# Kernel optimization log

Hardware: AMD Instinct MI355X
Metric: run time of the kernel (lower is better)

Reference implementation:

```python
import jax, jax.numpy as jnp
import numpy as np

TOP_K = 2


def setup_inputs() -> dict:
    key = jax.random.key(0)
    k1, k2, k3, k4, k5 = jax.random.split(key, 5)
    B, S, H, F, E = 2, 2048, 1024, 4096, 8
    scale = 0.02
    return {
        "hidden_states": jax.random.normal(k1, (B, S, H), dtype=jnp.float32),
        "w_gate": jax.random.normal(k2, (H, E), dtype=jnp.float32) * scale,
        "w_gate_proj": jax.random.normal(k3, (E, H, F), dtype=jnp.float32) * scale,
        "w_up_proj": jax.random.normal(k4, (E, H, F), dtype=jnp.float32) * scale,
        "w_down_proj": jax.random.normal(k5, (E, F, H), dtype=jnp.float32) * scale,
    }


def reference(hidden_states, w_gate, w_gate_proj, w_up_proj, w_down_proj):
    B, S, H = hidden_states.shape
    E = w_gate_proj.shape[0]
    x = hidden_states.reshape(-1, H)  # [T, H]

    # Router: softmax in float32, then top-k (NOT renormalized, matching source).
    router_logits = x @ w_gate  # [T, E]
    routing_probs = jax.nn.softmax(router_logits.astype(jnp.float32), axis=-1)
    routing_weights, selected_experts = jax.lax.top_k(routing_probs, TOP_K)  # [T, k]
    routing_weights = routing_weights.astype(x.dtype)

    out = jnp.zeros_like(x)
    # Small fixed loop over experts; per-token weight is zero for unrouted
    # tokens, so the masked dense computation is mathematically identical to
    # the gather/index_add dispatch in the source.
    for e in range(E):
        w_e = jnp.sum(routing_weights * (selected_experts == e), axis=-1)  # [T]
        h = jax.nn.silu(x @ w_gate_proj[e]) * (x @ w_up_proj[e])  # [T, F]
        out = out + (h @ w_down_proj[e]) * w_e[:, None]
    return out.reshape(B, S, H)
```

## Files before the change

kernel.cpp:

```cpp
#include <hip/hip_runtime.h>
#include <hip/hip_bf16.h>

#define T_TOK 4096
#define HDIM  1024
#define FDIM  4096
#define NEXP  8
#define CAP   4096
#define MAXWL 128
#define OBR   (2 * T_TOK + 128)

typedef __attribute__((ext_vector_type(8))) short short8;
typedef __attribute__((ext_vector_type(4))) float floatx4;
typedef __attribute__((ext_vector_type(4))) float float4v;
typedef __attribute__((ext_vector_type(4))) unsigned short ushort4v;

__device__ __forceinline__ unsigned short f2bf(float f) {
    union { float f; unsigned int u; } v; v.f = f;
    unsigned int u = v.u;
    u += 0x7fffu + ((u >> 16) & 1u);
    return (unsigned short)(u >> 16);
}

__device__ __forceinline__ void gl2lds16(const void* g, void* l) {
    __builtin_amdgcn_global_load_lds(
        (const __attribute__((address_space(1))) unsigned int*)g,
        (__attribute__((address_space(3))) unsigned int*)l,
        16, 0, 0);
}

__global__ void k_transpose_cast(const float* __restrict__ src, unsigned short* __restrict__ dst,
                                 int R, int C) {
    __shared__ float tile[64][65];
    size_t base = (size_t)blockIdx.z * (size_t)R * (size_t)C;
    int c0 = blockIdx.x * 64, r0 = blockIdx.y * 64;
    int lx = threadIdx.x & 15, ly = threadIdx.x >> 4;
#pragma unroll
    for (int i = 0; i < 4; ++i) {
        int rr = i * 16 + ly;
        float4v v = *(const float4v*)(src + base + (size_t)(r0 + rr) * C + c0 + lx * 4);
        tile[rr][lx * 4 + 0] = v[0]; tile[rr][lx * 4 + 1] = v[1];
        tile[rr][lx * 4 + 2] = v[2]; tile[rr][lx * 4 + 3] = v[3];
    }
    __syncthreads();
#pragma unroll
    for (int i = 0; i < 4; ++i) {
        int cc = i * 16 + ly;
        ushort4v o = { f2bf(tile[lx * 4 + 0][cc]), f2bf(tile[lx * 4 + 1][cc]),
                       f2bf(tile[lx * 4 + 2][cc]), f2bf(tile[lx * 4 + 3][cc]) };
        *(ushort4v*)(dst + base + (size_t)(c0 + cc) * R + r0 + lx * 4) = o;
    }
}

__global__ void k_router(const float* __restrict__ x, const float* __restrict__ wgate,
                         unsigned short* __restrict__ xb,
                         int* __restrict__ counts, int* __restrict__ ltok,
                         float* __restrict__ lwt, int* __restrict__ tslot) {
    int lane = threadIdx.x & 63;
    int tok = blockIdx.x * 4 + (threadIdx.x >> 6);
    const float* xr = x + (size_t)tok * HDIM;
    unsigned short* xbr = xb + (size_t)tok * HDIM;
    float acc[NEXP];
#pragma unroll
    for (int e = 0; e < NEXP; ++e) acc[e] = 0.f;
    for (int it = 0; it < HDIM / 256; ++it) {
        int h0 = it * 256 + lane * 4;
        float4v xv = *(const float4v*)(xr + h0);
        ushort4v xo = { f2bf(xv[0]), f2bf(xv[1]), f2bf(xv[2]), f2bf(xv[3]) };
        *(ushort4v*)(xbr + h0) = xo;
#pragma unroll
        for (int j = 0; j < 4; ++j) {
            float4v w0 = *(const float4v*)(wgate + (size_t)(h0 + j) * NEXP);
            float4v w1 = *(const float4v*)(wgate + (size_t)(h0 + j) * NEXP + 4);
            float xs = xv[j];
            acc[0] += xs * w0[0]; acc[1] += xs * w0[1];
            acc[2] += xs * w0[2]; acc[3] += xs * w0[3];
            acc[4] += xs * w1[0]; acc[5] += xs * w1[1];
            acc[6] += xs * w1[2]; acc[7] += xs * w1[3];
        }
    }
#pragma unroll
    for (int off = 32; off >= 1; off >>= 1)
#pragma unroll
        for (int e = 0; e < NEXP; ++e)
            acc[e] += __shfl_xor(acc[e], off, 64);
    if (lane == 0) {
        float m = acc[0];
#pragma unroll
        for (int e = 1; e < NEXP; ++e) m = fmaxf(m, acc[e]);
        float p[NEXP], s = 0.f;
#pragma unroll
        for (int e = 0; e < NEXP; ++e) { p[e] = __expf(acc[e] - m); s += p[e]; }
        float inv = 1.f / s;
#pragma unroll
        for (int e = 0; e < NEXP; ++e) p[e] *= inv;
        int e0 = 0; float b0 = p[0];
#pragma unroll
        for (int e = 1; e < NEXP; ++e) if (p[e] > b0) { b0 = p[e]; e0 = e; }
        int e1 = -1; float b1 = -1.f;
#pragma unroll
        for (int e = 0; e < NEXP; ++e) if (e != e0 && p[e] > b1) { b1 = p[e]; e1 = e; }
        int p0 = atomicAdd(&counts[e0], 1);
        ltok[e0 * CAP + p0] = tok; lwt[e0 * CAP + p0] = b0;
        int p1 = atomicAdd(&counts[e1], 1);
        ltok[e1 * CAP + p1] = tok; lwt[e1 * CAP + p1] = b1;
        tslot[tok * 2]     = (e0 << 16) | p0;
        tslot[tok * 2 + 1] = (e1 << 16) | p1;
    }
}

__global__ void k_prefix(const int* __restrict__ counts, int* __restrict__ offs,
                         int* __restrict__ wl, int* __restrict__ nwl) {
    if (threadIdx.x == 0) {
        int s = 0;
#pragma unroll
        for (int e = 0; e < NEXP; ++e) { offs[e] = s; s += counts[e]; }
        int n = 0;
        for (int e = 0; e < NEXP; ++e)
            for (int r = 0; r * 128 < counts[e] && n < MAXWL; ++r)
                wl[n++] = (e << 8) | r;
        nwl[0] = n;
    }
}

__global__ __launch_bounds__(256, 4)
void k_gemm1(const unsigned short* __restrict__ xb,
             const unsigned short* __restrict__ wgt,
             const unsigned short* __restrict__ wut,
             const int* __restrict__ counts, const int* __restrict__ offs,
             const int* __restrict__ ltok,
             const int* __restrict__ wl, const int* __restrict__ nwl,
             unsigned short* __restrict__ hbuf)
{
    if ((int)blockIdx.y >= nwl[0]) return;
    const int w = wl[blockIdx.y];
    const int e = w >> 8, rowtile = w & 255;
    const int M = counts[e];
    const int ftile = blockIdx.x;

    __shared__ __align__(16) unsigned short lA[128 * 32];
    __shared__ __align__(16) unsigned short lBg[64 * 32];
    __shared__ __align__(16) unsigned short lBu[64 * 32];
    __shared__ int stok[128];

    const int t = threadIdx.x;
    const int wave = t >> 6, lane = t & 63;

    if (t < 128) {
        int i = rowtile * 128 + t;
        stok[t] = (i < M) ? ltok[e * CAP + i] : ltok[e * CAP];
    }
    __syncthreads();

    const int r0 = t >> 2, k8 = t & 3;
    const unsigned short* pA0 = xb + (size_t)stok[r0] * HDIM + k8 * 8;
    const unsigned short* pA1 = xb + (size_t)stok[r0 + 64] * HDIM + k8 * 8;
    const size_t wbase = (size_t)e * FDIM * HDIM + (size_t)(ftile * 64) * HDIM;
    const unsigned short* pG0 = wgt + wbase + (size_t)r0 * HDIM + k8 * 8;
    const unsigned short* pU0 = wut + wbase + (size_t)r0 * HDIM + k8 * 8;

    unsigned short* dA0 = &lA[wave * 512];
    unsigned short* dA1 = &lA[2048 + wave * 512];
    unsigned short* dG0 = &lBg[wave * 512];
    unsigned short* dU0 = &lBu[wave * 512];

    const int wm = wave >> 1, wn = wave & 1;
    const int fr = lane & 15, kg = lane >> 4;

    floatx4 accg[4][2], accu[4][2];
#pragma unroll
    for (int mi = 0; mi < 4; ++mi)
#pragma unroll
        for (int ni = 0; ni < 2; ++ni) {
            floatx4 z = {0.f, 0.f, 0.f, 0.f};
            accg[mi][ni] = z; accu[mi][ni] = z;
        }

    for (int ks = 0; ks < HDIM / 32; ++ks) {
        gl2lds16(pA0, dA0); gl2lds16(pA1, dA1);
        gl2lds16(pG0, dG0); gl2lds16(pU0, dU0);
        pA0 += 32; pA1 += 32; pG0 += 32; pU0 += 32;
        __syncthreads();
        short8 a[4], bg[2], bu[2];
#pragma unroll
        for (int mi = 0; mi < 4; ++mi)
            a[mi] = *(const short8*)&lA[(wm * 64 + mi * 16 + fr) * 32 + kg * 8];
#pragma unroll
        for (int ni = 0; ni < 2; ++ni) {
            bg[ni] = *(const short8*)&lBg[(wn * 32 + ni * 16 + fr) * 32 + kg * 8];
            bu[ni] = *(const short8*)&lBu[(wn * 32 + ni * 16 + fr) * 32 + kg * 8];
        }
#pragma unroll
        for (int mi = 0; mi < 4; ++mi)
#pragma unroll
            for (int ni = 0; ni < 2; ++ni) {
                accg[mi][ni] = __builtin_amdgcn_mfma_f32_16x16x32_bf16(a[mi], bg[ni], accg[mi][ni], 0, 0, 0);
                accu[mi][ni] = __builtin_amdgcn_mfma_f32_16x16x32_bf16(a[mi], bu[ni], accu[mi][ni], 0, 0, 0);
            }
        __syncthreads();
    }

    const int hrow0 = offs[e] + rowtile * 128;
#pragma unroll
    for (int mi = 0; mi < 4; ++mi)
#pragma unroll
        for (int ni = 0; ni < 2; ++ni) {
            int c = ftile * 64 + wn * 32 + ni * 16 + fr;
#pragma unroll
            for (int r = 0; r < 4; ++r) {
                int rr = wm * 64 + mi * 16 + kg * 4 + r;
                if (rowtile * 128 + rr < M) {
                    float g = accg[mi][ni][r];
                    float val = (g / (1.f + __expf(-g))) * accu[mi][ni][r];
                    hbuf[(size_t)(hrow0 + rr) * FDIM + c] = f2bf(val);
                }
            }
        }
}

__global__ __launch_bounds__(256, 2)
void k_gemm2(const unsigned short* __restrict__ hbuf,
             const unsigned short* __restrict__ wdt,
             const int* __restrict__ counts, const int* __restrict__ offs,
             const float* __restrict__ lwt,
             const int* __restrict__ wl, const int* __restrict__ nwl,
             float* __restrict__ obuf)
{
    if ((int)blockIdx.y >= nwl[0]) return;
    const int w = wl[blockIdx.y];
    const int e = w >> 8, rowtile = w & 255;
    const int M = counts[e];
    const int htile = blockIdx.x;
    const int khalf = blockIdx.z;

    __shared__ __align__(16) unsigned short lA[128 * 32];
    __shared__ __align__(16) unsigned short lB[128 * 32];
    __shared__ float swt[128];

    const int t = threadIdx.x;
    const int wave = t >> 6, lane = t & 63;

    if (t < 128) {
        int i = rowtile * 128 + t;
        swt[t] = (i < M) ? lwt[e * CAP + i] : 0.f;
    }

    const int row0 = offs[e] + rowtile * 128;
    const int r0 = t >> 2, k8 = t & 3;
    const int kofs = khalf * (FDIM / 2);
    const unsigned short* pA0 = hbuf + (size_t)(row0 + r0) * FDIM + kofs + k8 * 8;
    const unsigned short* pA1 = hbuf + (size_t)(row0 + 64 + r0) * FDIM + kofs + k8 * 8;
    const size_t wb = (size_t)e * HDIM * FDIM + (size_t)(htile * 128) * FDIM;
    const unsigned short* pB0 = wdt + wb + (size_t)r0 * FDIM + kofs + k8 * 8;
    const unsigned short* pB1 = wdt + wb + (size_t)(64 + r0) * FDIM + kofs + k8 * 8;

    unsigned short* dA0 = &lA[wave * 512];
    unsigned short* dA1 = &lA[2048 + wave * 512];
    unsigned short* dB0 = &lB[wave * 512];
    unsigned short* dB1 = &lB[2048 + wave * 512];

    const int wm = wave >> 1, wn = wave & 1;
    const int fr = lane & 15, kg = lane >> 4;

    floatx4 acc[4][4];
#pragma unroll
    for (int mi = 0; mi < 4; ++mi)
#pragma unroll
        for (int ni = 0; ni < 4; ++ni) {
            floatx4 z = {0.f, 0.f, 0.f, 0.f};
            acc[mi][ni] = z;
        }

    for (int ks = 0; ks < FDIM / 64; ++ks) {
        gl2lds16(pA0, dA0); gl2lds16(pA1, dA1);
        gl2lds16(pB0, dB0); gl2lds16(pB1, dB1);
        pA0 += 32; pA1 += 32; pB0 += 32; pB1 += 32;
        __syncthreads();
        short8 a[4], b[4];
#pragma unroll
        for (int mi = 0; mi < 4; ++mi)
            a[mi] = *(const short8*)&lA[(wm * 64 + mi * 16 + fr) * 32 + kg * 8];
#pragma unroll
        for (int ni = 0; ni < 4; ++ni)
            b[ni] = *(const short8*)&lB[(wn * 64 + ni * 16 + fr) * 32 + kg * 8];
#pragma unroll
        for (int mi = 0; mi < 4; ++mi)
#pragma unroll
            for (int ni = 0; ni < 4; ++ni)
                acc[mi][ni] = __builtin_amdgcn_mfma_f32_16x16x32_bf16(a[mi], b[ni], acc[mi][ni], 0, 0, 0);
        __syncthreads();
    }

    float* ob = obuf + (size_t)khalf * OBR * HDIM;
#pragma unroll
    for (int mi = 0; mi < 4; ++mi)
#pragma unroll
        for (int ni = 0; ni < 4; ++ni) {
            int c = htile * 128 + wn * 64 + ni * 16 + fr;
#pragma unroll
            for (int r = 0; r < 4; ++r) {
                int rr = wm * 64 + mi * 16 + kg * 4 + r;
                if (rowtile * 128 + rr < M)
                    ob[(size_t)(row0 + rr) * HDIM + c] = acc[mi][ni][r] * swt[rr];
            }
        }
}

__global__ void k_combine(const float* __restrict__ obuf, const int* __restrict__ tslot,
                          const int* __restrict__ offs, float* __restrict__ out) {
    int gid = blockIdx.x * 256 + threadIdx.x;
    int tok = gid >> 8;
    int c = (gid & 255) * 4;
    int s0 = tslot[tok * 2], s1 = tslot[tok * 2 + 1];
    size_t r0 = (size_t)(offs[s0 >> 16] + (s0 & 0xFFFF));
    size_t r1 = (size_t)(offs[s1 >> 16] + (s1 & 0xFFFF));
    float4v v00 = *(const float4v*)(obuf + r0 * HDIM + c);
    float4v v01 = *(const float4v*)(obuf + ((size_t)OBR + r0) * HDIM + c);
    float4v v10 = *(const float4v*)(obuf + r1 * HDIM + c);
    float4v v11 = *(const float4v*)(obuf + ((size_t)OBR + r1) * HDIM + c);
    float4v s = v00 + v01 + v10 + v11;
    *(float4v*)(out + (size_t)tok * HDIM + c) = s;
}

extern "C" void kernel_launch(void* const* d_in, const int* in_sizes, int n_in,
                              void* d_out, int out_size, void* d_ws, size_t ws_size,
                              hipStream_t stream) {
    const float* x     = (const float*)d_in[0];
    const float* wgate = (const float*)d_in[1];
    const float* wg    = (const float*)d_in[2];
    const float* wu    = (const float*)d_in[3];
    const float* wd    = (const float*)d_in[4];
    float* out = (float*)d_out;

    char* ws = (char*)d_ws;
    size_t off = 0;
    unsigned short* xb  = (unsigned short*)(ws + off); off += (size_t)T_TOK * HDIM * 2;
    unsigned short* wgt = (unsigned short*)(ws + off); off += (size_t)NEXP * FDIM * HDIM * 2;
    unsigned short* wut = (unsigned short*)(ws + off); off += (size_t)NEXP * FDIM * HDIM * 2;
    unsigned short* wdt = (unsigned short*)(ws + off); off += (size_t)NEXP * HDIM * FDIM * 2;
    unsigned short* hbuf= (unsigned short*)(ws + off); off += (size_t)OBR * FDIM * 2;
    int*   ltok   = (int*)(ws + off);   off += (size_t)NEXP * CAP * 4;
    float* lwt    = (float*)(ws + off); off += (size_t)NEXP * CAP * 4;
    int*   tslot  = (int*)(ws + off);   off += (size_t)T_TOK * 2 * 4;
    int*   counts = (int*)(ws + off);   off += 256;
    int*   offs   = (int*)(ws + off);   off += 256;
    int*   wl     = (int*)(ws + off);   off += MAXWL * 4;
    int*   nwl    = (int*)(ws + off);   off += 256;
    float* obuf = (float*)wgt;

    hipMemsetAsync(counts, 0, 32, stream);

    k_router<<<T_TOK / 4, 256, 0, stream>>>(x, wgate, xb, counts, ltok, lwt, tslot);
    k_transpose_cast<<<dim3(FDIM / 64, HDIM / 64, NEXP), 256, 0, stream>>>(wg, wgt, HDIM, FDIM);
    k_transpose_cast<<<dim3(FDIM / 64, HDIM / 64, NEXP), 256, 0, stream>>>(wu, wut, HDIM, FDIM);
    k_transpose_cast<<<dim3(HDIM / 64, FDIM / 64, NEXP), 256, 0, stream>>>(wd, wdt, FDIM, HDIM);
    k_prefix<<<1, 64, 0, stream>>>(counts, offs, wl, nwl);
    k_gemm1<<<dim3(FDIM / 64, 72), 256, 0, stream>>>(xb, wgt, wut, counts, offs, ltok, wl, nwl, hbuf);
    k_gemm2<<<dim3(HDIM / 128, 72, 2), 256, 0, stream>>>(hbuf, wdt, counts, offs, lwt, wl, nwl, obuf);
    k_combine<<<T_TOK * HDIM / 1024, 256, 0, stream>>>(obuf, tslot, offs, out);
}
```

Baseline: 832.9 us.

## Rewrite gate/up GEMM with 256-row tiles, triple-buffered swizzled LDS pipeline

The first expert GEMM now uses 512-thread blocks over 256-token row tiles with a 64-wide K step. Global-to-LDS copies are triple-buffered and split into two phases that overlap with MFMA work, controlled by explicit vmcnt waits, raw barriers and setprio. LDS rows are XOR-swizzled to avoid bank conflicts. A separate 256-row worklist is built in the prefix kernel. The intent is more reuse of weight tiles and hidden load latency, at the cost of much more LDS per block and lower occupancy.

Result: slower. 879.4 us (+5.6%).

```diff
diff --git a/kernel.cpp b/kernel.cpp
--- a/kernel.cpp
+++ b/kernel.cpp
@@ -7,12 +7,17 @@
 #define NEXP  8
 #define CAP   4096
 #define MAXWL 128
+#define NT1MAX 40
 #define OBR   (2 * T_TOK + 128)
 
 typedef __attribute__((ext_vector_type(8))) short short8;
 typedef __attribute__((ext_vector_type(4))) float floatx4;
 typedef __attribute__((ext_vector_type(4))) float float4v;
 typedef __attribute__((ext_vector_type(4))) unsigned short ushort4v;
+
+#define BAR() do { asm volatile("" ::: "memory"); __builtin_amdgcn_s_barrier(); asm volatile("" ::: "memory"); } while (0)
+#define VMW6() asm volatile("s_waitcnt vmcnt(6)" ::: "memory")
+#define VMW0() asm volatile("s_waitcnt vmcnt(0)" ::: "memory")
 
 __device__ __forceinline__ unsigned short f2bf(float f) {
     union { float f; unsigned int u; } v; v.f = f;
@@ -109,7 +114,8 @@
 }
 
 __global__ void k_prefix(const int* __restrict__ counts, int* __restrict__ offs,
-                         int* __restrict__ wl, int* __restrict__ nwl) {
+                         int* __restrict__ wl, int* __restrict__ nwl,
+                         int* __restrict__ wl1, int* __restrict__ nwl1) {
     if (threadIdx.x == 0) {
         int s = 0;
 #pragma unroll
@@ -119,52 +125,64 @@
             for (int r = 0; r * 128 < counts[e] && n < MAXWL; ++r)
                 wl[n++] = (e << 8) | r;
         nwl[0] = n;
-    }
-}
-
-__global__ __launch_bounds__(256, 4)
+        int n1 = 0;
+        for (int e = 0; e < NEXP; ++e)
+            for (int r = 0; r * 256 < counts[e] && n1 < 64; ++r)
+                wl1[n1++] = (e << 8) | r;
+        nwl1[0] = n1;
+    }
+}
+
+__global__ __launch_bounds__(512, 2)
 void k_gemm1(const unsigned short* __restrict__ xb,
              const unsigned short* __restrict__ wgt,
              const unsigned short* __restrict__ wut,
              const int* __restrict__ counts, const int* __restrict__ offs,
              const int* __restrict__ ltok,
-             const int* __restrict__ wl, const int* __restrict__ nwl,
+             const int* __restrict__ wl1, const int* __restrict__ nwl1,
              unsigned short* __restrict__ hbuf)
 {
-    if ((int)blockIdx.y >= nwl[0]) return;
-    const int w = wl[blockIdx.y];
-    const int e = w >> 8, rowtile = w & 255;
+    if ((int)blockIdx.y >= nwl1[0]) return;
+    const int wle = wl1[blockIdx.y];
+    const int e = wle >> 8, rowtile = wle & 255;
     const int M = counts[e];
     const int ftile = blockIdx.x;
 
-    __shared__ __align__(16) unsigned short lA[128 * 32];
-    __shared__ __align__(16) unsigned short lBg[64 * 32];
-    __shared__ __align__(16) unsigned short lBu[64 * 32];
-    __shared__ int stok[128];
+    __shared__ __align__(16) unsigned short lA[3][256 * 64];
+    __shared__ __align__(16) unsigned short lBg[3][64 * 64];
+    __shared__ __align__(16) unsigned short lBu[3][64 * 64];
+    __shared__ int stok[256];
 
     const int t = threadIdx.x;
     const int wave = t >> 6, lane = t & 63;
-
-    if (t < 128) {
-        int i = rowtile * 128 + t;
-        stok[t] = (i < M) ? ltok[e * CAP + i] : ltok[e * CAP];
-    }
-    __syncthreads();
-
-    const int r0 = t >> 2, k8 = t & 3;
-    const unsigned short* pA0 = xb + (size_t)stok[r0] * HDIM + k8 * 8;
-    const unsigned short* pA1 = xb + (size_t)stok[r0 + 64] * HDIM + k8 * 8;
-    const size_t wbase = (size_t)e * FDIM * HDIM + (size_t)(ftile * 64) * HDIM;
-    const unsigned short* pG0 = wgt + wbase + (size_t)r0 * HDIM + k8 * 8;
-    const unsigned short* pU0 = wut + wbase + (size_t)r0 * HDIM + k8 * 8;
-
-    unsigned short* dA0 = &lA[wave * 512];
-    unsigned short* dA1 = &lA[2048 + wave * 512];
-    unsigned short* dG0 = &lBg[wave * 512];
-    unsigned short* dU0 = &lBu[wave * 512];
-
     const int wm = wave >> 1, wn = wave & 1;
     const int fr = lane & 15, kg = lane >> 4;
+    const int fr7 = fr & 7;
+    const int w8 = wave * 8;
+    const int lr = lane >> 3, lc = lane & 7;
+    const int swz = (lc ^ lr) * 8;
+
+    if (t < 256) {
+        int i = rowtile * 256 + t;
+        stok[t] = (i < M) ? ltok[e * CAP + i] : ltok[e * CAP];
+    }
+    __syncthreads();
+
+    const unsigned short* pa0 = xb + (size_t)stok[  0 + w8 + lr] * HDIM + swz;
+    const unsigned short* pa1 = xb + (size_t)stok[ 64 + w8 + lr] * HDIM + swz;
+    const unsigned short* pa2 = xb + (size_t)stok[128 + w8 + lr] * HDIM + swz;
+    const unsigned short* pa3 = xb + (size_t)stok[192 + w8 + lr] * HDIM + swz;
+    const size_t wrow = (size_t)(e * FDIM + ftile * 64 + w8 + lr) * HDIM + swz;
+    const unsigned short* pg = wgt + wrow;
+    const unsigned short* pu = wut + wrow;
+
+    int ar[4], br[2];
+#pragma unroll
+    for (int mi = 0; mi < 4; ++mi) ar[mi] = (wm * 64 + mi * 16 + fr) * 64;
+#pragma unroll
+    for (int ni = 0; ni < 2; ++ni) br[ni] = (wn * 32 + ni * 16 + fr) * 64;
+    const int cs0 = ((0 + kg) ^ fr7) * 8;
+    const int cs1 = ((4 + kg) ^ fr7) * 8;
 
     floatx4 accg[4][2], accu[4][2];
 #pragma unroll
@@ -175,31 +193,90 @@
             accg[mi][ni] = z; accu[mi][ni] = z;
         }
 
-    for (int ks = 0; ks < HDIM / 32; ++ks) {
-        gl2lds16(pA0, dA0); gl2lds16(pA1, dA1);
-        gl2lds16(pG0, dG0); gl2lds16(pU0, dU0);
-        pA0 += 32; pA1 += 32; pG0 += 32; pU0 += 32;
-        __syncthreads();
-        short8 a[4], bg[2], bu[2];
-#pragma unroll
-        for (int mi = 0; mi < 4; ++mi)
-            a[mi] = *(const short8*)&lA[(wm * 64 + mi * 16 + fr) * 32 + kg * 8];
+    auto stage_tile = [&](int b) {
+        unsigned short* sA = &lA[b][0];
+        gl2lds16(pa0, sA + (  0 + w8) * 64); pa0 += 64;
+        gl2lds16(pa1, sA + ( 64 + w8) * 64); pa1 += 64;
+        gl2lds16(pa2, sA + (128 + w8) * 64); pa2 += 64;
+        gl2lds16(pa3, sA + (192 + w8) * 64); pa3 += 64;
+        gl2lds16(pg, &lBg[b][w8 * 64]); pg += 64;
+        gl2lds16(pu, &lBu[b][w8 * 64]); pu += 64;
+    };
+
+    auto do_tile = [&](int cur, int stb, bool dostage) {
+        const unsigned short* cA = &lA[cur][0];
+        const unsigned short* cG = &lBg[cur][0];
+        const unsigned short* cU = &lBu[cur][0];
+        unsigned short* sA = &lA[stb][0];
+        short8 a[4], g[2], u[2];
+#pragma unroll
+        for (int mi = 0; mi < 4; ++mi) a[mi] = *(const short8*)(cA + ar[mi] + cs0);
 #pragma unroll
         for (int ni = 0; ni < 2; ++ni) {
-            bg[ni] = *(const short8*)&lBg[(wn * 32 + ni * 16 + fr) * 32 + kg * 8];
-            bu[ni] = *(const short8*)&lBu[(wn * 32 + ni * 16 + fr) * 32 + kg * 8];
-        }
-#pragma unroll
-        for (int mi = 0; mi < 4; ++mi)
-#pragma unroll
-            for (int ni = 0; ni < 2; ++ni) {
-                accg[mi][ni] = __builtin_amdgcn_mfma_f32_16x16x32_bf16(a[mi], bg[ni], accg[mi][ni], 0, 0, 0);
-                accu[mi][ni] = __builtin_amdgcn_mfma_f32_16x16x32_bf16(a[mi], bu[ni], accu[mi][ni], 0, 0, 0);
-            }
-        __syncthreads();
-    }
-
-    const int hrow0 = offs[e] + rowtile * 128;
+            g[ni] = *(const short8*)(cG + br[ni] + cs0);
+            u[ni] = *(const short8*)(cU + br[ni] + cs0);
+        }
+        if (dostage) {
+            gl2lds16(pa0, sA + (  0 + w8) * 64); pa0 += 64;
+            gl2lds16(pa1, sA + ( 64 + w8) * 64); pa1 += 64;
+            gl2lds16(pg, &lBg[stb][w8 * 64]); pg += 64;
+        }
+        BAR();
+        __builtin_amdgcn_s_setprio(1);
+#pragma unroll
+        for (int mi = 0; mi < 4; ++mi)
+#pragma unroll
+            for (int ni = 0; ni < 2; ++ni)
+                accg[mi][ni] = __builtin_amdgcn_mfma_f32_16x16x32_bf16(a[mi], g[ni], accg[mi][ni], 0, 0, 0);
+#pragma unroll
+        for (int mi = 0; mi < 4; ++mi)
+#pragma unroll
+            for (int ni = 0; ni < 2; ++ni)
+                accu[mi][ni] = __builtin_amdgcn_mfma_f32_16x16x32_bf16(a[mi], u[ni], accu[mi][ni], 0, 0, 0);
+        __builtin_amdgcn_s_setprio(0);
+        BAR();
+#pragma unroll
+        for (int mi = 0; mi < 4; ++mi) a[mi] = *(const short8*)(cA + ar[mi] + cs1);
+#pragma unroll
+        for (int ni = 0; ni < 2; ++ni) {
+            g[ni] = *(const short8*)(cG + br[ni] + cs1);
+            u[ni] = *(const short8*)(cU + br[ni] + cs1);
+        }
+        if (dostage) {
+            gl2lds16(pa2, sA + (128 + w8) * 64); pa2 += 64;
+            gl2lds16(pa3, sA + (192 + w8) * 64); pa3 += 64;
+            gl2lds16(pu, &lBu[stb][w8 * 64]); pu += 64;
+        }
+        BAR();
+        __builtin_amdgcn_s_setprio(1);
+#pragma unroll
+        for (int mi = 0; mi < 4; ++mi)
+#pragma unroll
+            for (int ni = 0; ni < 2; ++ni)
+                accg[mi][ni] = __builtin_amdgcn_mfma_f32_16x16x32_bf16(a[mi], g[ni], accg[mi][ni], 0, 0, 0);
+#pragma unroll
+        for (int mi = 0; mi < 4; ++mi)
+#pragma unroll
+            for (int ni = 0; ni < 2; ++ni)
+                accu[mi][ni] = __builtin_amdgcn_mfma_f32_16x16x32_bf16(a[mi], u[ni], accu[mi][ni], 0, 0, 0);
+        __builtin_amdgcn_s_setprio(0);
+    };
+
+    stage_tile(0);
+    stage_tile(1);
+    VMW6();
+    BAR();
+
+    int cur = 0, st = 2;
+    for (int kt = 0; kt < 16; ++kt) {
+        do_tile(cur, st, kt < 14);
+        if (kt < 14) { VMW6(); } else { VMW0(); }
+        BAR();
+        cur = (cur == 2) ? 0 : cur + 1;
+        st  = (st  == 2) ? 0 : st  + 1;
+    }
+
+    const int hrow0 = offs[e] + rowtile * 256;
 #pragma unroll
     for (int mi = 0; mi < 4; ++mi)
 #pragma unroll
@@ -208,9 +285,9 @@
 #pragma unroll
             for (int r = 0; r < 4; ++r) {
                 int rr = wm * 64 + mi * 16 + kg * 4 + r;
-                if (rowtile * 128 + rr < M) {
-                    float g = accg[mi][ni][r];
-                    float val = (g / (1.f + __expf(-g))) * accu[mi][ni][r];
+                if (rowtile * 256 + rr < M) {
+                    float gv = accg[mi][ni][r];
+                    float val = (gv / (1.f + __expf(-gv))) * accu[mi][ni][r];
                     hbuf[(size_t)(hrow0 + rr) * FDIM + c] = f2bf(val);
                 }
             }
@@ -345,6 +422,8 @@
     int*   offs   = (int*)(ws + off);   off += 256;
     int*   wl     = (int*)(ws + off);   off += MAXWL * 4;
     int*   nwl    = (int*)(ws + off);   off += 256;
+    int*   wl1    = (int*)(ws + off);   off += 64 * 4;
+    int*   nwl1   = (int*)(ws + off);   off += 256;
     float* obuf = (float*)wgt;
 
     hipMemsetAsync(counts, 0, 32, stream);
@@ -353,8 +432,8 @@
     k_transpose_cast<<<dim3(FDIM / 64, HDIM / 64, NEXP), 256, 0, stream>>>(wg, wgt, HDIM, FDIM);
     k_transpose_cast<<<dim3(FDIM / 64, HDIM / 64, NEXP), 256, 0, stream>>>(wu, wut, HDIM, FDIM);
     k_transpose_cast<<<dim3(HDIM / 64, FDIM / 64, NEXP), 256, 0, stream>>>(wd, wdt, FDIM, HDIM);
-    k_prefix<<<1, 64, 0, stream>>>(counts, offs, wl, nwl);
-    k_gemm1<<<dim3(FDIM / 64, 72), 256, 0, stream>>>(xb, wgt, wut, counts, offs, ltok, wl, nwl, hbuf);
+    k_prefix<<<1, 64, 0, stream>>>(counts, offs, wl, nwl, wl1, nwl1);
+    k_gemm1<<<dim3(FDIM / 64, NT1MAX), 512, 0, stream>>>(xb, wgt, wut, counts, offs, ltok, wl1, nwl1, hbuf);
     k_gemm2<<<dim3(HDIM / 128, 72, 2), 256, 0, stream>>>(hbuf, wdt, counts, offs, lwt, wl, nwl, obuf);
     k_combine<<<T_TOK * HDIM / 1024, 256, 0, stream>>>(obuf, tslot, offs, out);
 }
```

## Double-buffer LDS tiles and XOR-swizzle K chunks in both MoE GEMMs

Applied to the files above, without the earlier changes.

Both expert GEMM kernels now keep two LDS buffers and issue the global-to-LDS loads for the next K step before computing on the current one. This is meant to overlap memory latency with MFMA work. It also XOR-swizzles the 8-element K chunk position by row on both the load and read sides, to cut LDS bank conflicts. In exchange, LDS use per block doubles, which may lower occupancy, and the 4-per-SM launch bound on gemm1 may no longer fit.

New measurement: 834.2 us. About the same (+0.2%).

```diff
diff --git a/kernel.cpp b/kernel.cpp
--- a/kernel.cpp
+++ b/kernel.cpp
@@ -137,9 +137,9 @@
     const int M = counts[e];
     const int ftile = blockIdx.x;
 
-    __shared__ __align__(16) unsigned short lA[128 * 32];
-    __shared__ __align__(16) unsigned short lBg[64 * 32];
-    __shared__ __align__(16) unsigned short lBu[64 * 32];
+    __shared__ __align__(16) unsigned short lA[2][128 * 32];
+    __shared__ __align__(16) unsigned short lBg[2][64 * 32];
+    __shared__ __align__(16) unsigned short lBu[2][64 * 32];
     __shared__ int stok[128];
 
     const int t = threadIdx.x;
@@ -152,19 +152,16 @@
     __syncthreads();
 
     const int r0 = t >> 2, k8 = t & 3;
-    const unsigned short* pA0 = xb + (size_t)stok[r0] * HDIM + k8 * 8;
-    const unsigned short* pA1 = xb + (size_t)stok[r0 + 64] * HDIM + k8 * 8;
+    const int sw0 = (k8 ^ ((r0 >> 1) & 3)) * 8;
+    const unsigned short* pA0 = xb + (size_t)stok[r0] * HDIM + sw0;
+    const unsigned short* pA1 = xb + (size_t)stok[r0 + 64] * HDIM + sw0;
     const size_t wbase = (size_t)e * FDIM * HDIM + (size_t)(ftile * 64) * HDIM;
-    const unsigned short* pG0 = wgt + wbase + (size_t)r0 * HDIM + k8 * 8;
-    const unsigned short* pU0 = wut + wbase + (size_t)r0 * HDIM + k8 * 8;
-
-    unsigned short* dA0 = &lA[wave * 512];
-    unsigned short* dA1 = &lA[2048 + wave * 512];
-    unsigned short* dG0 = &lBg[wave * 512];
-    unsigned short* dU0 = &lBu[wave * 512];
+    const unsigned short* pG0 = wgt + wbase + (size_t)r0 * HDIM + sw0;
+    const unsigned short* pU0 = wut + wbase + (size_t)r0 * HDIM + sw0;
 
     const int wm = wave >> 1, wn = wave & 1;
     const int fr = lane & 15, kg = lane >> 4;
+    const int cswz = (kg ^ ((fr >> 1) & 3)) * 8;
 
     floatx4 accg[4][2], accu[4][2];
 #pragma unroll
@@ -175,27 +172,40 @@
             accg[mi][ni] = z; accu[mi][ni] = z;
         }
 
-    for (int ks = 0; ks < HDIM / 32; ++ks) {
-        gl2lds16(pA0, dA0); gl2lds16(pA1, dA1);
-        gl2lds16(pG0, dG0); gl2lds16(pU0, dU0);
-        pA0 += 32; pA1 += 32; pG0 += 32; pU0 += 32;
+    auto stage = [&](int b) {
+        gl2lds16(pA0, &lA[b][wave * 512]);        pA0 += 32;
+        gl2lds16(pA1, &lA[b][2048 + wave * 512]); pA1 += 32;
+        gl2lds16(pG0, &lBg[b][wave * 512]);       pG0 += 32;
+        gl2lds16(pU0, &lBu[b][wave * 512]);       pU0 += 32;
+    };
+    auto compute = [&](int b) {
+        short8 a[4], g[2], u[2];
+#pragma unroll
+        for (int mi = 0; mi < 4; ++mi)
+            a[mi] = *(const short8*)&lA[b][(wm * 64 + mi * 16 + fr) * 32 + cswz];
+#pragma unroll
+        for (int ni = 0; ni < 2; ++ni) {
+            g[ni] = *(const short8*)&lBg[b][(wn * 32 + ni * 16 + fr) * 32 + cswz];
+            u[ni] = *(const short8*)&lBu[b][(wn * 32 + ni * 16 + fr) * 32 + cswz];
+        }
+#pragma unroll
+        for (int mi = 0; mi < 4; ++mi)
+#pragma unroll
+            for (int ni = 0; ni < 2; ++ni) {
+                accg[mi][ni] = __builtin_amdgcn_mfma_f32_16x16x32_bf16(a[mi], g[ni], accg[mi][ni], 0, 0, 0);
+                accu[mi][ni] = __builtin_amdgcn_mfma_f32_16x16x32_bf16(a[mi], u[ni], accu[mi][ni], 0, 0, 0);
+            }
+    };
+
+    stage(0);
+    __syncthreads();
+#pragma unroll 1
+    for (int it = 0; it < 16; ++it) {
+        stage(1);
+        compute(0);
         __syncthreads();
-        short8 a[4], bg[2], bu[2];
-#pragma unroll
-        for (int mi = 0; mi < 4; ++mi)
-            a[mi] = *(const short8*)&lA[(wm * 64 + mi * 16 + fr) * 32 + kg * 8];
-#pragma unroll
-        for (int ni = 0; ni < 2; ++ni) {
-            bg[ni] = *(const short8*)&lBg[(wn * 32 + ni * 16 + fr) * 32 + kg * 8];
-            bu[ni] = *(const short8*)&lBu[(wn * 32 + ni * 16 + fr) * 32 + kg * 8];
-        }
-#pragma unroll
-        for (int mi = 0; mi < 4; ++mi)
-#pragma unroll
-            for (int ni = 0; ni < 2; ++ni) {
-                accg[mi][ni] = __builtin_amdgcn_mfma_f32_16x16x32_bf16(a[mi], bg[ni], accg[mi][ni], 0, 0, 0);
-                accu[mi][ni] = __builtin_amdgcn_mfma_f32_16x16x32_bf16(a[mi], bu[ni], accu[mi][ni], 0, 0, 0);
-            }
+        if (it < 15) stage(0);
+        compute(1);
         __syncthreads();
     }
 
@@ -232,8 +242,8 @@
     const int htile = blockIdx.x;
     const int khalf = blockIdx.z;
 
-    __shared__ __align__(16) unsigned short lA[128 * 32];
-    __shared__ __align__(16) unsigned short lB[128 * 32];
+    __shared__ __align__(16) unsigned short lA[2][128 * 32];
+    __shared__ __align__(16) unsigned short lB[2][128 * 32];
     __shared__ float swt[128];
 
     const int t = threadIdx.x;
@@ -247,19 +257,16 @@
     const int row0 = offs[e] + rowtile * 128;
     const int r0 = t >> 2, k8 = t & 3;
     const int kofs = khalf * (FDIM / 2);
-    const unsigned short* pA0 = hbuf + (size_t)(row0 + r0) * FDIM + kofs + k8 * 8;
-    const unsigned short* pA1 = hbuf + (size_t)(row0 + 64 + r0) * FDIM + kofs + k8 * 8;
+    const int sw0 = (k8 ^ ((r0 >> 1) & 3)) * 8;
+    const unsigned short* pA0 = hbuf + (size_t)(row0 + r0) * FDIM + kofs + sw0;
+    const unsigned short* pA1 = hbuf + (size_t)(row0 + 64 + r0) * FDIM + kofs + sw0;
     const size_t wb = (size_t)e * HDIM * FDIM + (size_t)(htile * 128) * FDIM;
-    const unsigned short* pB0 = wdt + wb + (size_t)r0 * FDIM + kofs + k8 * 8;
-    const unsigned short* pB1 = wdt + wb + (size_t)(64 + r0) * FDIM + kofs + k8 * 8;
-
-    unsigned short* dA0 = &lA[wave * 512];
-    unsigned short* dA1 = &lA[2048 + wave * 512];
-    unsigned short* dB0 = &lB[wave * 512];
-    unsigned short* dB1 = &lB[2048 + wave * 512];
+    const unsigned short* pB0 = wdt + wb + (size_t)r0 * FDIM + kofs + sw0;
+    const unsigned short* pB1 = wdt + wb + (size_t)(64 + r0) * FDIM + kofs + sw0;
 
     const int wm = wave >> 1, wn = wave & 1;
     const int fr = lane & 15, kg = lane >> 4;
+    const int cswz = (kg ^ ((fr >> 1) & 3)) * 8;
 
     floatx4 acc[4][4];
 #pragma unroll
@@ -270,23 +277,36 @@
             acc[mi][ni] = z;
         }
 
-    for (int ks = 0; ks < FDIM / 64; ++ks) {
-        gl2lds16(pA0, dA0); gl2lds16(pA1, dA1);
-        gl2lds16(pB0, dB0); gl2lds16(pB1, dB1);
-        pA0 += 32; pA1 += 32; pB0 += 32; pB1 += 32;
+    auto stage = [&](int b) {
+        gl2lds16(pA0, &lA[b][wave * 512]);        pA0 += 32;
+        gl2lds16(pA1, &lA[b][2048 + wave * 512]); pA1 += 32;
+        gl2lds16(pB0, &lB[b][wave * 512]);        pB0 += 32;
+        gl2lds16(pB1, &lB[b][2048 + wave * 512]); pB1 += 32;
+    };
+    auto compute = [&](int b) {
+        short8 a[4], bb[4];
+#pragma unroll
+        for (int mi = 0; mi < 4; ++mi)
+            a[mi] = *(const short8*)&lA[b][(wm * 64 + mi * 16 + fr) * 32 + cswz];
+#pragma unroll
+        for (int ni = 0; ni < 4; ++ni)
+            bb[ni] = *(const short8*)&lB[b][(wn * 64 + ni * 16 + fr) * 32 + cswz];
+#pragma unroll
+        for (int mi = 0; mi < 4; ++mi)
+#pragma unroll
+            for (int ni = 0; ni < 4; ++ni)
+                acc[mi][ni] = __builtin_amdgcn_mfma_f32_16x16x32_bf16(a[mi], bb[ni], acc[mi][ni], 0, 0, 0);
+    };
+
+    stage(0);
+    __syncthreads();
+#pragma unroll 1
+    for (int it = 0; it < 32; ++it) {
+        stage(1);
+        compute(0);
         __syncthreads();
-        short8 a[4], b[4];
-#pragma unroll
-        for (int mi = 0; mi < 4; ++mi)
-            a[mi] = *(const short8*)&lA[(wm * 64 + mi * 16 + fr) * 32 + kg * 8];
-#pragma unroll
-        for (int ni = 0; ni < 4; ++ni)
-            b[ni] = *(const short8*)&lB[(wn * 64 + ni * 16 + fr) * 32 + kg * 8];
-#pragma unroll
-        for (int mi = 0; mi < 4; ++mi)
-#pragma unroll
-            for (int ni = 0; ni < 4; ++ni)
-                acc[mi][ni] = __builtin_amdgcn_mfma_f32_16x16x32_bf16(a[mi], b[ni], acc[mi][ni], 0, 0, 0);
+        if (it < 31) stage(0);
+        compute(1);
         __syncthreads();
     }
 
```
